# Performance work log

Measured on AMD Instinct MI355X. Metric: run time of the kernel, lower is better.

Reference implementation:

```python
import jax, jax.numpy as jnp
import numpy as np

B, T, DI, H = 64, 512, 512, 1024


def setup_inputs() -> dict:
    key = jax.random.key(0)
    k1, k2, k3, k4 = jax.random.split(key, 4)
    inputs = jax.random.normal(k1, (B, T, DI), dtype=jnp.float32)
    # PyTorch LSTMCell params: weight_ih (4H, Di) kaiming-normal, weight_hh (4H, H) orthogonal-ish,
    # bias_hh = 0, bias_ih = 0 except forget-gate chunk = 1 (gate order: i, f, g, o).
    W_ih = jax.random.normal(k2, (4 * H, DI), dtype=jnp.float32) * np.float32((2.0 / DI) ** 0.5)
    W_hh = jax.random.normal(k3, (4 * H, H), dtype=jnp.float32) * np.float32((1.0 / H) ** 0.5)
    b_ih = jnp.concatenate([jnp.zeros((H,)), jnp.ones((H,)), jnp.zeros((2 * H,))]).astype(jnp.float32)
    b_hh = jnp.zeros((4 * H,), dtype=jnp.float32)
    length = jax.random.randint(k4, (B,), 1, T + 1, dtype=jnp.int32)
    return {"inputs": inputs, "W_ih": W_ih, "W_hh": W_hh, "b_ih": b_ih, "b_hh": b_hh, "length": length}


def reference(inputs, W_ih, W_hh, b_ih, b_hh, length):
    Bn, Tn, _ = inputs.shape
    Hn = W_hh.shape[1]
    # Precompute input projection for all timesteps in one big GEMM (same math, fewer launches).
    x_proj = jnp.einsum('btd,gd->btg', inputs, W_ih) + (b_ih + b_hh)  # (B, T, 4H)

    def step(carry, xp_t):
        h, c = carry
        gates = xp_t + h @ W_hh.T  # (B, 4H)
        i, f, g, o = jnp.split(gates, 4, axis=-1)
        c_new = jax.nn.sigmoid(f) * c + jax.nn.sigmoid(i) * jnp.tanh(g)
        h_new = jax.nn.sigmoid(o) * jnp.tanh(c_new)
        return (h_new, c_new), (h_new, c_new)

    h0 = jnp.zeros((Bn, Hn), dtype=inputs.dtype)
    c0 = jnp.zeros((Bn, Hn), dtype=inputs.dtype)
    _, (hs, cs) = jax.lax.scan(step, (h0, c0), jnp.moveaxis(x_proj, 1, 0))
    hs = jnp.moveaxis(hs, 0, 1)  # (B, T, H)
    cs = jnp.moveaxis(cs, 0, 1)  # (B, T, H)
    idx = length - 1
    bidx = jnp.arange(Bn)
    h_last = hs[bidx, idx]  # (B, H)
    c_last = cs[bidx, idx]  # (B, H)
    return (hs, cs, h_last, c_last)
```

## Files before the change

### kernel.cpp

```cpp
#include <hip/hip_runtime.h>

#define B_   64
#define T_   512
#define DI_  512
#define H_   1024
#define G4H  4096
#define KQ   8
#define BKQ  (H_ / KQ)

__device__ __forceinline__ float sigm(float x) {
    return 1.0f / (1.0f + __expf(-x));
}
__device__ __forceinline__ float tanh_fast(float x) {
    return 2.0f / (1.0f + __expf(-2.0f * x)) - 1.0f;
}

__global__ __launch_bounds__(256) void transpose_whh(
    const float* __restrict__ Whh, float* __restrict__ WT)
{
    __shared__ float tile[64][65];
    const int r0 = blockIdx.x * 64;
    const int k0 = blockIdx.y * 64;
    const int tid = threadIdx.x;
    const int lx = tid & 63;
    const int ly = tid >> 6;
#pragma unroll
    for (int i = 0; i < 64; i += 4)
        tile[ly + i][lx] = Whh[(size_t)(r0 + ly + i) * H_ + k0 + lx];
    __syncthreads();
#pragma unroll
    for (int i = 0; i < 64; i += 4)
        WT[(size_t)(k0 + ly + i) * G4H + r0 + lx] = tile[lx][ly + i];
}

__global__ __launch_bounds__(256) void xproj_gemm(
    const float* __restrict__ X, const float* __restrict__ Wih,
    const float* __restrict__ bih, const float* __restrict__ bhh,
    float* __restrict__ xp, int t0)
{
    __shared__ float As[16][64];
    __shared__ float Bs[16][64];
    const int tl = blockIdx.y;
    const int n0 = blockIdx.x * 64;
    const int t  = t0 + tl;
    const int tid = threadIdx.x;
    const int ab = tid >> 2;
    const int ak = (tid & 3) * 4;
    const int wn = tid >> 2;
    const int wk = (tid & 3) * 4;
    const int by = tid >> 4;
    const int nx = tid & 15;

    const float* Ap = X + ((size_t)ab * T_ + t) * DI_ + ak;
    const float* Bp = Wih + (size_t)(n0 + wn) * DI_ + wk;

    float acc[4][4] = {};

    for (int k0 = 0; k0 < DI_; k0 += 16) {
        const float4 av = *(const float4*)(Ap + k0);
        const float4 bv = *(const float4*)(Bp + k0);
        __syncthreads();
        As[ak + 0][ab] = av.x; As[ak + 1][ab] = av.y;
        As[ak + 2][ab] = av.z; As[ak + 3][ab] = av.w;
        Bs[wk + 0][wn] = bv.x; Bs[wk + 1][wn] = bv.y;
        Bs[wk + 2][wn] = bv.z; Bs[wk + 3][wn] = bv.w;
        __syncthreads();
#pragma unroll
        for (int k = 0; k < 16; ++k) {
            const float4 a4 = *(const float4*)&As[k][by * 4];
            const float4 b4 = *(const float4*)&Bs[k][nx * 4];
            const float ar[4] = {a4.x, a4.y, a4.z, a4.w};
            const float br[4] = {b4.x, b4.y, b4.z, b4.w};
#pragma unroll
            for (int i = 0; i < 4; ++i)
#pragma unroll
                for (int j = 0; j < 4; ++j)
                    acc[i][j] = fmaf(ar[i], br[j], acc[i][j]);
        }
    }

    const int nb = n0 + nx * 4;
    const float4 b1 = *(const float4*)(bih + nb);
    const float4 b2 = *(const float4*)(bhh + nb);
    const float4 bb4 = {b1.x + b2.x, b1.y + b2.y, b1.z + b2.z, b1.w + b2.w};
#pragma unroll
    for (int i = 0; i < 4; ++i) {
        const int b = by * 4 + i;
        float4 v;
        v.x = acc[i][0] + bb4.x;
        v.y = acc[i][1] + bb4.y;
        v.z = acc[i][2] + bb4.z;
        v.w = acc[i][3] + bb4.w;
        *(float4*)(xp + ((size_t)tl * B_ + b) * G4H + nb) = v;
    }
}

__global__ __launch_bounds__(256) void step_gemm(
    const float* __restrict__ WT, const float* __restrict__ h,
    float* __restrict__ part)
{
    __shared__ float As[16][64];
    __shared__ float Bs[16][64];
    const int n0    = blockIdx.x * 64;
    const int kbase = blockIdx.y * BKQ;
    const int tid = threadIdx.x;
    const int ab = tid >> 2;
    const int ak = (tid & 3) * 4;
    const int bk = tid >> 4;
    const int bn = (tid & 15) * 4;
    const int by = tid >> 4;
    const int nx = tid & 15;

    const float* Ap = h + (size_t)ab * H_ + kbase + ak;
    const float* Bp = WT + (size_t)(kbase + bk) * G4H + n0 + bn;

    float acc[4][4] = {};

    for (int k0 = 0; k0 < BKQ; k0 += 16) {
        const float4 av = *(const float4*)(Ap + k0);
        const float4 bv = *(const float4*)(Bp + (size_t)k0 * G4H);
        __syncthreads();
        As[ak + 0][ab] = av.x; As[ak + 1][ab] = av.y;
        As[ak + 2][ab] = av.z; As[ak + 3][ab] = av.w;
        *(float4*)&Bs[bk][bn] = bv;
        __syncthreads();
#pragma unroll
        for (int k = 0; k < 16; ++k) {
            const float4 a4 = *(const float4*)&As[k][by * 4];
            const float4 b4 = *(const float4*)&Bs[k][nx * 4];
            const float ar[4] = {a4.x, a4.y, a4.z, a4.w};
            const float br[4] = {b4.x, b4.y, b4.z, b4.w};
#pragma unroll
            for (int i = 0; i < 4; ++i)
#pragma unroll
                for (int j = 0; j < 4; ++j)
                    acc[i][j] = fmaf(ar[i], br[j], acc[i][j]);
        }
    }

    float* P = part + (size_t)blockIdx.y * B_ * G4H;
#pragma unroll
    for (int i = 0; i < 4; ++i) {
        const int b = by * 4 + i;
        float4 v = {acc[i][0], acc[i][1], acc[i][2], acc[i][3]};
        *(float4*)(P + (size_t)b * G4H + n0 + nx * 4) = v;
    }
}

__global__ __launch_bounds__(128) void lstm_point(
    const float* __restrict__ part, const float* __restrict__ xp,
    float* __restrict__ h, float* __restrict__ cT,
    float* __restrict__ hs, float* __restrict__ cs, int tl, int t)
{
    const int gi = blockIdx.x * 128 + threadIdx.x;
    const int b  = gi >> 8;
    const int j  = (gi & 255) * 4;

    const float* xpb = xp + ((size_t)tl * B_ + b) * G4H;
    float4 g0 = *(const float4*)(xpb + j);
    float4 g1 = *(const float4*)(xpb + H_ + j);
    float4 g2 = *(const float4*)(xpb + 2 * H_ + j);
    float4 g3 = *(const float4*)(xpb + 3 * H_ + j);
#pragma unroll
    for (int p = 0; p < KQ; ++p) {
        const float* P = part + ((size_t)p * B_ + b) * G4H;
        const float4 a = *(const float4*)(P + j);
        const float4 f = *(const float4*)(P + H_ + j);
        const float4 g = *(const float4*)(P + 2 * H_ + j);
        const float4 o = *(const float4*)(P + 3 * H_ + j);
        g0.x += a.x; g0.y += a.y; g0.z += a.z; g0.w += a.w;
        g1.x += f.x; g1.y += f.y; g1.z += f.z; g1.w += f.w;
        g2.x += g.x; g2.y += g.y; g2.z += g.z; g2.w += g.w;
        g3.x += o.x; g3.y += o.y; g3.z += o.z; g3.w += o.w;
    }

    const size_t sidx = (size_t)b * H_ + j;
    const float4 cp = *(const float4*)(cT + sidx);
    float cn[4], hn[4];
    const float ii[4] = {g0.x, g0.y, g0.z, g0.w};
    const float ff[4] = {g1.x, g1.y, g1.z, g1.w};
    const float gg[4] = {g2.x, g2.y, g2.z, g2.w};
    const float oo[4] = {g3.x, g3.y, g3.z, g3.w};
    const float cc[4] = {cp.x, cp.y, cp.z, cp.w};
#pragma unroll
    for (int q = 0; q < 4; ++q) {
        const float c2 = fmaf(sigm(ff[q]), cc[q], sigm(ii[q]) * tanh_fast(gg[q]));
        cn[q] = c2;
        hn[q] = sigm(oo[q]) * tanh_fast(c2);
    }
    const float4 cv = {cn[0], cn[1], cn[2], cn[3]};
    const float4 hv = {hn[0], hn[1], hn[2], hn[3]};
    *(float4*)(cT + sidx) = cv;
    *(float4*)(h + sidx) = hv;
    const size_t oidx = ((size_t)b * T_ + t) * H_ + j;
    *(float4*)(hs + oidx) = hv;
    *(float4*)(cs + oidx) = cv;
}

__global__ __launch_bounds__(256) void gather_last(
    const float* __restrict__ hs, const float* __restrict__ cs,
    const int* __restrict__ length,
    float* __restrict__ hl, float* __restrict__ cl)
{
    const int i = blockIdx.x * 256 + threadIdx.x;
    const int b = i >> 10;
    const int j = i & 1023;
    const int tt = length[b] - 1;
    const size_t src = ((size_t)b * T_ + tt) * H_ + j;
    hl[i] = hs[src];
    cl[i] = cs[src];
}

extern "C" void kernel_launch(void* const* d_in, const int* in_sizes, int n_in,
                              void* d_out, int out_size, void* d_ws, size_t ws_size,
                              hipStream_t stream)
{
    const float* X   = (const float*)d_in[0];
    const float* Wih = (const float*)d_in[1];
    const float* Whh = (const float*)d_in[2];
    const float* bih = (const float*)d_in[3];
    const float* bhh = (const float*)d_in[4];
    const int*   len = (const int*)d_in[5];

    float* out = (float*)d_out;
    float* hs = out;
    float* cs = hs + (size_t)B_ * T_ * H_;
    float* hl = cs + (size_t)B_ * T_ * H_;
    float* cl = hl + (size_t)B_ * H_;

    float* h    = (float*)d_ws;
    float* cT   = h + (size_t)B_ * H_;
    float* WT   = cT + (size_t)B_ * H_;
    float* part = WT + (size_t)H_ * G4H;
    float* xp   = part + (size_t)KQ * B_ * G4H;

    const size_t fixed_bytes =
        ((size_t)2 * B_ * H_ + (size_t)H_ * G4H + (size_t)KQ * B_ * G4H) * sizeof(float);
    const size_t per_t = (size_t)B_ * G4H * sizeof(float);

    int Tc = 1;
    if (ws_size > fixed_bytes + per_t) {
        size_t m = (ws_size - fixed_bytes) / per_t;
        Tc = (int)(m > (size_t)T_ ? (size_t)T_ : m);
    }

    hipMemsetAsync(h, 0, (size_t)2 * B_ * H_ * sizeof(float), stream);
    transpose_whh<<<dim3(64, 16), 256, 0, stream>>>(Whh, WT);

    for (int t0 = 0; t0 < T_; t0 += Tc) {
        const int clen = (T_ - t0 < Tc) ? (T_ - t0) : Tc;
        xproj_gemm<<<dim3(G4H / 64, clen), 256, 0, stream>>>(X, Wih, bih, bhh, xp, t0);
        for (int tl = 0; tl < clen; ++tl) {
            const int t = t0 + tl;
            step_gemm<<<dim3(64, KQ), 256, 0, stream>>>(WT, h, part);
            lstm_point<<<128, 128, 0, stream>>>(part, xp, h, cT, hs, cs, tl, t);
        }
    }
    gather_last<<<(B_ * H_) / 256, 256, 0, stream>>>(hs, cs, len, hl, cl);
}
```

Measured before the change: 11.12 ms.

## Replace per-step GEMM and pointwise launches with persistent cooperative recurrence kernel

Replaces the two kernel launches per timestep (split-K step GEMM writing partials, then a pointwise reduce) with one persistent cooperative kernel of 256 blocks. Each block owns 4 hidden units across all four gates and keeps its packed W_hh slice streaming from a block-contiguous layout. Gate reduction happens in shared memory via atomics, the LSTM cell update is fused in, and timesteps are separated by grid.sync. This removes launch overhead and the round-trip of partial sums through global memory, at the cost of a grid-wide barrier per step and needing all blocks co-resident.

Result: slower. 31.58 ms (+184.0%).

```diff
diff --git a/kernel.cpp b/kernel.cpp
--- a/kernel.cpp
+++ b/kernel.cpp
@@ -1,12 +1,13 @@
 #include <hip/hip_runtime.h>
+#include <hip/hip_cooperative_groups.h>
+
+namespace cg = cooperative_groups;
 
 #define B_   64
 #define T_   512
 #define DI_  512
 #define H_   1024
 #define G4H  4096
-#define KQ   8
-#define BKQ  (H_ / KQ)
 
 __device__ __forceinline__ float sigm(float x) {
     return 1.0f / (1.0f + __expf(-x));
@@ -15,22 +16,26 @@
     return 2.0f / (1.0f + __expf(-2.0f * x)) - 1.0f;
 }
 
-__global__ __launch_bounds__(256) void transpose_whh(
-    const float* __restrict__ Whh, float* __restrict__ WT)
-{
-    __shared__ float tile[64][65];
-    const int r0 = blockIdx.x * 64;
-    const int k0 = blockIdx.y * 64;
+__global__ __launch_bounds__(256) void pack_whh(
+    const float* __restrict__ Whh, float* __restrict__ Wpk)
+{
+    const int bid = blockIdx.x;
+    const int j0  = bid * 4;
     const int tid = threadIdx.x;
-    const int lx = tid & 63;
-    const int ly = tid >> 6;
-#pragma unroll
-    for (int i = 0; i < 64; i += 4)
-        tile[ly + i][lx] = Whh[(size_t)(r0 + ly + i) * H_ + k0 + lx];
-    __syncthreads();
-#pragma unroll
-    for (int i = 0; i < 64; i += 4)
-        WT[(size_t)(k0 + ly + i) * G4H + r0 + lx] = tile[lx][ly + i];
+    const int n   = tid >> 4;
+    const int lo  = tid & 15;
+    const int row = (n >> 2) * H_ + j0 + (n & 3);
+    const float* src = Whh + (size_t)row * H_;
+    float* dst = Wpk + (size_t)bid * 16384 + n;
+#pragma unroll
+    for (int u = 0; u < 16; ++u) {
+        const int k = u * 64 + lo * 4;
+        const float4 v = *(const float4*)(src + k);
+        dst[(size_t)(k + 0) * 16] = v.x;
+        dst[(size_t)(k + 1) * 16] = v.y;
+        dst[(size_t)(k + 2) * 16] = v.z;
+        dst[(size_t)(k + 3) * 16] = v.w;
+    }
 }
 
 __global__ __launch_bounds__(256) void xproj_gemm(
@@ -95,106 +100,126 @@
     }
 }
 
-__global__ __launch_bounds__(256) void step_gemm(
-    const float* __restrict__ WT, const float* __restrict__ h,
-    float* __restrict__ part)
-{
-    __shared__ float As[16][64];
-    __shared__ float Bs[16][64];
-    const int n0    = blockIdx.x * 64;
-    const int kbase = blockIdx.y * BKQ;
+__global__ __launch_bounds__(512, 2) void lstm_recur(
+    const float* __restrict__ Wpk, const float* __restrict__ xp,
+    float* __restrict__ hT, float* __restrict__ cS,
+    float* __restrict__ hs, float* __restrict__ cs,
+    int t0, int clen)
+{
+    __shared__ float Hs[2][4096];
+    __shared__ float Wt[2][1280];
+    __shared__ float gate[64 * 21];
+    __shared__ float hloc[256];
+
     const int tid = threadIdx.x;
-    const int ab = tid >> 2;
-    const int ak = (tid & 3) * 4;
-    const int bk = tid >> 4;
-    const int bn = (tid & 15) * 4;
-    const int by = tid >> 4;
-    const int nx = tid & 15;
-
-    const float* Ap = h + (size_t)ab * H_ + kbase + ak;
-    const float* Bp = WT + (size_t)(kbase + bk) * G4H + n0 + bn;
-
-    float acc[4][4] = {};
-
-    for (int k0 = 0; k0 < BKQ; k0 += 16) {
-        const float4 av = *(const float4*)(Ap + k0);
-        const float4 bv = *(const float4*)(Bp + (size_t)k0 * G4H);
-        __syncthreads();
-        As[ak + 0][ab] = av.x; As[ak + 1][ab] = av.y;
-        As[ak + 2][ab] = av.z; As[ak + 3][ab] = av.w;
-        *(float4*)&Bs[bk][bn] = bv;
-        __syncthreads();
-#pragma unroll
-        for (int k = 0; k < 16; ++k) {
-            const float4 a4 = *(const float4*)&As[k][by * 4];
-            const float4 b4 = *(const float4*)&Bs[k][nx * 4];
-            const float ar[4] = {a4.x, a4.y, a4.z, a4.w};
-            const float br[4] = {b4.x, b4.y, b4.z, b4.w};
-#pragma unroll
-            for (int i = 0; i < 4; ++i)
-#pragma unroll
-                for (int j = 0; j < 4; ++j)
-                    acc[i][j] = fmaf(ar[i], br[j], acc[i][j]);
-        }
-    }
-
-    float* P = part + (size_t)blockIdx.y * B_ * G4H;
-#pragma unroll
-    for (int i = 0; i < 4; ++i) {
-        const int b = by * 4 + i;
-        float4 v = {acc[i][0], acc[i][1], acc[i][2], acc[i][3]};
-        *(float4*)(P + (size_t)b * G4H + n0 + nx * 4) = v;
-    }
-}
-
-__global__ __launch_bounds__(128) void lstm_point(
-    const float* __restrict__ part, const float* __restrict__ xp,
-    float* __restrict__ h, float* __restrict__ cT,
-    float* __restrict__ hs, float* __restrict__ cs, int tl, int t)
-{
-    const int gi = blockIdx.x * 128 + threadIdx.x;
-    const int b  = gi >> 8;
-    const int j  = (gi & 255) * 4;
-
-    const float* xpb = xp + ((size_t)tl * B_ + b) * G4H;
-    float4 g0 = *(const float4*)(xpb + j);
-    float4 g1 = *(const float4*)(xpb + H_ + j);
-    float4 g2 = *(const float4*)(xpb + 2 * H_ + j);
-    float4 g3 = *(const float4*)(xpb + 3 * H_ + j);
-#pragma unroll
-    for (int p = 0; p < KQ; ++p) {
-        const float* P = part + ((size_t)p * B_ + b) * G4H;
-        const float4 a = *(const float4*)(P + j);
-        const float4 f = *(const float4*)(P + H_ + j);
-        const float4 g = *(const float4*)(P + 2 * H_ + j);
-        const float4 o = *(const float4*)(P + 3 * H_ + j);
-        g0.x += a.x; g0.y += a.y; g0.z += a.z; g0.w += a.w;
-        g1.x += f.x; g1.y += f.y; g1.z += f.z; g1.w += f.w;
-        g2.x += g.x; g2.y += g.y; g2.z += g.z; g2.w += g.w;
-        g3.x += o.x; g3.y += o.y; g3.z += o.z; g3.w += o.w;
-    }
-
-    const size_t sidx = (size_t)b * H_ + j;
-    const float4 cp = *(const float4*)(cT + sidx);
-    float cn[4], hn[4];
-    const float ii[4] = {g0.x, g0.y, g0.z, g0.w};
-    const float ff[4] = {g1.x, g1.y, g1.z, g1.w};
-    const float gg[4] = {g2.x, g2.y, g2.z, g2.w};
-    const float oo[4] = {g3.x, g3.y, g3.z, g3.w};
-    const float cc[4] = {cp.x, cp.y, cp.z, cp.w};
-#pragma unroll
-    for (int q = 0; q < 4; ++q) {
-        const float c2 = fmaf(sigm(ff[q]), cc[q], sigm(ii[q]) * tanh_fast(gg[q]));
-        cn[q] = c2;
-        hn[q] = sigm(oo[q]) * tanh_fast(c2);
-    }
-    const float4 cv = {cn[0], cn[1], cn[2], cn[3]};
-    const float4 hv = {hn[0], hn[1], hn[2], hn[3]};
-    *(float4*)(cT + sidx) = cv;
-    *(float4*)(h + sidx) = hv;
-    const size_t oidx = ((size_t)b * T_ + t) * H_ + j;
-    *(float4*)(hs + oidx) = hv;
-    *(float4*)(cs + oidx) = cv;
+    const int bid = blockIdx.x;
+    const int j0  = bid * 4;
+    const float* Wb = Wpk + (size_t)bid * 16384;
+
+    const int wv = tid >> 6;
+    const int ln = tid & 63;
+    const int b4 = ln >> 2;
+    const int n4 = ln & 3;
+
+    cg::grid_group grid = cg::this_grid();
+
+    for (int tl = 0; tl < clen; ++tl) {
+        const int t = t0 + tl;
+
+        {
+            const float4 a0 = *(const float4*)(hT + tid * 4);
+            const float4 a1 = *(const float4*)(hT + 2048 + tid * 4);
+            *(float4*)(&Hs[0][tid * 4])        = a0;
+            *(float4*)(&Hs[0][2048 + tid * 4]) = a1;
+        }
+        if (tid < 256) {
+            const float4 w = *(const float4*)(Wb + tid * 4);
+            *(float4*)(&Wt[0][(tid >> 2) * 20 + (tid & 3) * 4]) = w;
+        } else {
+            const int q = tid - 256;
+            const int b = q >> 2, g = q & 3;
+            const float4 v = *(const float4*)(xp + ((size_t)tl * B_ + b) * G4H + g * H_ + j0);
+            float* gp = gate + b * 21 + g * 4;
+            gp[0] = v.x; gp[1] = v.y; gp[2] = v.z; gp[3] = v.w;
+        }
+        __syncthreads();
+
+        float acc[4][4] = {};
+        for (int kt = 0; kt < 16; ++kt) {
+            const int buf = kt & 1;
+            float4 r0, r1, w4;
+            if (kt < 15) {
+                const float* hsrc = hT + (kt + 1) * 4096;
+                r0 = *(const float4*)(hsrc + tid * 4);
+                r1 = *(const float4*)(hsrc + 2048 + tid * 4);
+                if (tid < 256)
+                    w4 = *(const float4*)(Wb + (size_t)(kt + 1) * 1024 + tid * 4);
+            }
+            const float* Hb   = &Hs[buf][0];
+            const float* Wrow = &Wt[buf][0];
+#pragma unroll
+            for (int kk = 0; kk < 8; ++kk) {
+                const int k = wv * 8 + kk;
+                const float4 hv = *(const float4*)(Hb + k * 64 + b4 * 4);
+                const float4 wq = *(const float4*)(Wrow + k * 20 + n4 * 4);
+                const float hr[4] = {hv.x, hv.y, hv.z, hv.w};
+                const float wr[4] = {wq.x, wq.y, wq.z, wq.w};
+#pragma unroll
+                for (int i = 0; i < 4; ++i)
+#pragma unroll
+                    for (int j = 0; j < 4; ++j)
+                        acc[i][j] = fmaf(hr[i], wr[j], acc[i][j]);
+            }
+            if (kt < 15) {
+                *(float4*)(&Hs[buf ^ 1][tid * 4])        = r0;
+                *(float4*)(&Hs[buf ^ 1][2048 + tid * 4]) = r1;
+                if (tid < 256)
+                    *(float4*)(&Wt[buf ^ 1][(tid >> 2) * 20 + (tid & 3) * 4]) = w4;
+                __syncthreads();
+            }
+        }
+
+#pragma unroll
+        for (int i = 0; i < 4; ++i)
+#pragma unroll
+            for (int j = 0; j < 4; ++j)
+                atomicAdd(&gate[(b4 * 4 + i) * 21 + n4 * 4 + j], acc[i][j]);
+        __syncthreads();
+
+        if (tid < 64) {
+            const int b = tid;
+            const float* gp = gate + b * 21;
+            const float4 cv = *(const float4*)(cS + (size_t)b * H_ + j0);
+            const float cc[4] = {cv.x, cv.y, cv.z, cv.w};
+            float cn[4], hn[4];
+#pragma unroll
+            for (int q = 0; q < 4; ++q) {
+                const float ig = sigm(gp[q]);
+                const float fg = sigm(gp[4 + q]);
+                const float gg = tanh_fast(gp[8 + q]);
+                const float og = sigm(gp[12 + q]);
+                const float c2 = fmaf(fg, cc[q], ig * gg);
+                cn[q] = c2;
+                hn[q] = og * tanh_fast(c2);
+            }
+            const float4 c4 = {cn[0], cn[1], cn[2], cn[3]};
+            const float4 h4 = {hn[0], hn[1], hn[2], hn[3]};
+            *(float4*)(cS + (size_t)b * H_ + j0) = c4;
+            const size_t o = ((size_t)b * T_ + t) * H_ + j0;
+            *(float4*)(hs + o) = h4;
+            *(float4*)(cs + o) = c4;
+            hloc[0 * 64 + b] = hn[0];
+            hloc[1 * 64 + b] = hn[1];
+            hloc[2 * 64 + b] = hn[2];
+            hloc[3 * 64 + b] = hn[3];
+        }
+        __syncthreads();
+        if (tid < 64) {
+            const int q = tid >> 4, x = tid & 15;
+            *(float4*)(hT + (j0 + q) * 64 + x * 4) = *(const float4*)(hloc + q * 64 + x * 4);
+        }
+        grid.sync();
+    }
 }
 
 __global__ __launch_bounds__(256) void gather_last(
@@ -228,14 +253,12 @@
     float* hl = cs + (size_t)B_ * T_ * H_;
     float* cl = hl + (size_t)B_ * H_;
 
-    float* h    = (float*)d_ws;
-    float* cT   = h + (size_t)B_ * H_;
-    float* WT   = cT + (size_t)B_ * H_;
-    float* part = WT + (size_t)H_ * G4H;
-    float* xp   = part + (size_t)KQ * B_ * G4H;
-
-    const size_t fixed_bytes =
-        ((size_t)2 * B_ * H_ + (size_t)H_ * G4H + (size_t)KQ * B_ * G4H) * sizeof(float);
+    float* hT  = (float*)d_ws;
+    float* cS  = hT + 65536;
+    float* Wpk = cS + 65536;
+    float* xp  = Wpk + (size_t)H_ * G4H;
+
+    const size_t fixed_bytes = ((size_t)131072 + (size_t)H_ * G4H) * sizeof(float);
     const size_t per_t = (size_t)B_ * G4H * sizeof(float);
 
     int Tc = 1;
@@ -244,17 +267,18 @@
         Tc = (int)(m > (size_t)T_ ? (size_t)T_ : m);
     }
 
-    hipMemsetAsync(h, 0, (size_t)2 * B_ * H_ * sizeof(float), stream);
-    transpose_whh<<<dim3(64, 16), 256, 0, stream>>>(Whh, WT);
+    hipMemsetAsync(hT, 0, (size_t)131072 * sizeof(float), stream);
+    pack_whh<<<256, 256, 0, stream>>>(Whh, Wpk);
 
     for (int t0 = 0; t0 < T_; t0 += Tc) {
         const int clen = (T_ - t0 < Tc) ? (T_ - t0) : Tc;
         xproj_gemm<<<dim3(G4H / 64, clen), 256, 0, stream>>>(X, Wih, bih, bhh, xp, t0);
-        for (int tl = 0; tl < clen; ++tl) {
-            const int t = t0 + tl;
-            step_gemm<<<dim3(64, KQ), 256, 0, stream>>>(WT, h, part);
-            lstm_point<<<128, 128, 0, stream>>>(part, xp, h, cT, hs, cs, tl, t);
-        }
-    }
+        int t0a = t0, cla = clen;
+        void* args[] = {(void*)&Wpk, (void*)&xp, (void*)&hT, (void*)&cS,
+                        (void*)&hs, (void*)&cs, (void*)&t0a, (void*)&cla};
+        hipLaunchCooperativeKernel((const void*)lstm_recur, dim3(256), dim3(512),
+                                   args, 0, stream);
+    }
+
     gather_last<<<(B_ * H_) / 256, 256, 0, stream>>>(hs, cs, len, hl, cl);
 }
```
